# Kernel tuning notes

Measured on AMD Instinct MI355X. Metric: run time of the kernel, lower is better.

## Reference

```python
import jax, jax.numpy as jnp
import numpy as np


def setup_inputs() -> dict:
    key = jax.random.key(0)
    kx, kb, kc, ka = jax.random.split(key, 4)
    batch, seq_len, state_dim = 4, 4096, 1024
    shape = (batch, seq_len, state_dim)
    x = jax.random.normal(kx, shape, dtype=jnp.float32)
    B = jax.random.normal(kb, shape, dtype=jnp.float32)
    C = jax.random.normal(kc, shape, dtype=jnp.float32)
    A = jax.random.uniform(ka, shape, dtype=jnp.float32)  # decay gates in (0,1)
    return {"x": x, "B": B, "C": C, "A": A}


def reference(x, B, C, A):
    # Diagonal selective-scan recurrence: h_t = A_t * h_{t-1} + B_t; y_t = C_t * h_t.
    # x is accepted for interface parity but unused (as in the original module).
    # Scan over time with carry h: [batch, state_dim].
    A_t = jnp.moveaxis(A, 1, 0)  # [seq, batch, dim]
    B_t = jnp.moveaxis(B, 1, 0)
    C_t = jnp.moveaxis(C, 1, 0)
    h0 = jnp.zeros((B.shape[0], B.shape[2]), dtype=B.dtype)

    def step(h, abc):
        a, b, c = abc
        h = a * h + b
        return h, c * h

    _, ys = jax.lax.scan(step, h0, (A_t, B_t, C_t))
    return jnp.moveaxis(ys, 0, 1)  # [batch, seq, dim]
```

## Files before the change

### kernel.cpp

```cpp
#include <hip/hip_runtime.h>

#define BATCH 4
#define SEQ   4096
#define DIM   1024
#define DIM4  (DIM / 4)
#define NC    128
#define CHUNK (SEQ / NC)

__device__ __forceinline__ float4 f4_fma(float4 a, float4 h, float4 b) {
    float4 r;
    r.x = fmaf(a.x, h.x, b.x);
    r.y = fmaf(a.y, h.y, b.y);
    r.z = fmaf(a.z, h.z, b.z);
    r.w = fmaf(a.w, h.w, b.w);
    return r;
}

__device__ __forceinline__ float4 f4_mul(float4 a, float4 b) {
    float4 r;
    r.x = a.x * b.x;
    r.y = a.y * b.y;
    r.z = a.z * b.z;
    r.w = a.w * b.w;
    return r;
}

__global__ __launch_bounds__(256) void ssm_phase1(const float4* __restrict__ A,
                                                  const float4* __restrict__ B,
                                                  float4* __restrict__ P,
                                                  float4* __restrict__ Q) {
    const int c  = blockIdx.x % NC;
    const int b  = blockIdx.x / NC;
    const int d4 = threadIdx.x;

    size_t base = ((size_t)b * SEQ + (size_t)c * CHUNK) * DIM4 + d4;

    float4 p = make_float4(1.f, 1.f, 1.f, 1.f);
    float4 q = make_float4(0.f, 0.f, 0.f, 0.f);

#pragma unroll 8
    for (int t = 0; t < CHUNK; ++t) {
        float4 a  = A[base + (size_t)t * DIM4];
        float4 bb = B[base + (size_t)t * DIM4];
        q = f4_fma(a, q, bb);
        p = f4_mul(p, a);
    }

    size_t w = ((size_t)b * NC + c) * DIM4 + d4;
    P[w] = p;
    Q[w] = q;
}

__global__ __launch_bounds__(256) void ssm_phase2(float4* __restrict__ PH,
                                                  const float4* __restrict__ Q) {
    const int gid = blockIdx.x * 256 + threadIdx.x;
    const int b   = gid / DIM4;
    const int d4  = gid % DIM4;

    float4 h = make_float4(0.f, 0.f, 0.f, 0.f);
    for (int c = 0; c < NC; ++c) {
        size_t idx = ((size_t)b * NC + c) * DIM4 + d4;
        float4 p = PH[idx];
        float4 q = Q[idx];
        PH[idx] = h;
        h = f4_fma(p, h, q);
    }
}

__global__ __launch_bounds__(256) void ssm_phase3(const float4* __restrict__ A,
                                                  const float4* __restrict__ B,
                                                  const float4* __restrict__ C,
                                                  const float4* __restrict__ H,
                                                  float4* __restrict__ Y) {
    const int c  = blockIdx.x % NC;
    const int b  = blockIdx.x / NC;
    const int d4 = threadIdx.x;

    size_t base = ((size_t)b * SEQ + (size_t)c * CHUNK) * DIM4 + d4;

    float4 h = H[((size_t)b * NC + c) * DIM4 + d4];

#pragma unroll 4
    for (int t = 0; t < CHUNK; ++t) {
        float4 a  = A[base + (size_t)t * DIM4];
        float4 bb = B[base + (size_t)t * DIM4];
        float4 cc = C[base + (size_t)t * DIM4];
        h = f4_fma(a, h, bb);
        Y[base + (size_t)t * DIM4] = f4_mul(cc, h);
    }
}

extern "C" void kernel_launch(void* const* d_in, const int* in_sizes, int n_in,
                              void* d_out, int out_size, void* d_ws, size_t ws_size,
                              hipStream_t stream) {
    const float* B = (const float*)d_in[1];
    const float* C = (const float*)d_in[2];
    const float* A = (const float*)d_in[3];
    float* Y = (float*)d_out;

    float* P = (float*)d_ws;
    float* Q = P + (size_t)BATCH * NC * DIM;

    ssm_phase1<<<BATCH * NC, 256, 0, stream>>>(
        (const float4*)A, (const float4*)B, (float4*)P, (float4*)Q);

    ssm_phase2<<<(BATCH * DIM4) / 256, 256, 0, stream>>>(
        (float4*)P, (const float4*)Q);

    ssm_phase3<<<BATCH * NC, 256, 0, stream>>>(
        (const float4*)A, (const float4*)B, (const float4*)C,
        (const float4*)P, (float4*)Y);
}
```

Measured before the change: 86.53 us.

## Use more chunks and a parallel Hillis-Steele scan for chunk carries

Result: slower. 95.29 us (+10.1%).

```diff
diff --git a/kernel.cpp b/kernel.cpp
--- a/kernel.cpp
+++ b/kernel.cpp
@@ -4,7 +4,7 @@
 #define SEQ   4096
 #define DIM   1024
 #define DIM4  (DIM / 4)
-#define NC    128
+#define NC    512
 #define CHUNK (SEQ / NC)
 
 __device__ __forceinline__ float4 f4_fma(float4 a, float4 h, float4 b) {
@@ -38,7 +38,7 @@
     float4 p = make_float4(1.f, 1.f, 1.f, 1.f);
     float4 q = make_float4(0.f, 0.f, 0.f, 0.f);
 
-#pragma unroll 8
+#pragma unroll
     for (int t = 0; t < CHUNK; ++t) {
         float4 a  = A[base + (size_t)t * DIM4];
         float4 bb = B[base + (size_t)t * DIM4];
@@ -51,20 +51,38 @@
     Q[w] = q;
 }
 
-__global__ __launch_bounds__(256) void ssm_phase2(float4* __restrict__ PH,
-                                                  const float4* __restrict__ Q) {
-    const int gid = blockIdx.x * 256 + threadIdx.x;
-    const int b   = gid / DIM4;
-    const int d4  = gid % DIM4;
+__global__ __launch_bounds__(NC) void ssm_phase2(float4* __restrict__ PH,
+                                                 const float4* __restrict__ Q) {
+    const int b  = blockIdx.x / DIM4;
+    const int d4 = blockIdx.x % DIM4;
+    const int c  = threadIdx.x;
 
-    float4 h = make_float4(0.f, 0.f, 0.f, 0.f);
-    for (int c = 0; c < NC; ++c) {
-        size_t idx = ((size_t)b * NC + c) * DIM4 + d4;
-        float4 p = PH[idx];
-        float4 q = Q[idx];
-        PH[idx] = h;
-        h = f4_fma(p, h, q);
+    __shared__ float4 sp[NC];
+    __shared__ float4 sq[NC];
+
+    const size_t idx = ((size_t)b * NC + c) * DIM4 + d4;
+    float4 p = PH[idx];
+    float4 q = Q[idx];
+    sp[c] = p;
+    sq[c] = q;
+    __syncthreads();
+
+    for (int off = 1; off < NC; off <<= 1) {
+        float4 pp, qq;
+        const bool has = (c >= off);
+        if (has) { pp = sp[c - off]; qq = sq[c - off]; }
+        __syncthreads();
+        if (has) {
+            q = f4_fma(p, qq, q);
+            p = f4_mul(p, pp);
+            sp[c] = p;
+            sq[c] = q;
+        }
+        __syncthreads();
     }
+
+    float4 h = (c == 0) ? make_float4(0.f, 0.f, 0.f, 0.f) : sq[c - 1];
+    PH[idx] = h;
 }
 
 __global__ __launch_bounds__(256) void ssm_phase3(const float4* __restrict__ A,
@@ -80,7 +98,7 @@
 
     float4 h = H[((size_t)b * NC + c) * DIM4 + d4];
 
-#pragma unroll 4
+#pragma unroll
     for (int t = 0; t < CHUNK; ++t) {
         float4 a  = A[base + (size_t)t * DIM4];
         float4 bb = B[base + (size_t)t * DIM4];
@@ -104,7 +122,7 @@
     ssm_phase1<<<BATCH * NC, 256, 0, stream>>>(
         (const float4*)A, (const float4*)B, (float4*)P, (float4*)Q);
 
-    ssm_phase2<<<(BATCH * DIM4) / 256, 256, 0, stream>>>(
+    ssm_phase2<<<BATCH * DIM4, NC, 0, stream>>>(
         (float4*)P, (const float4*)Q);
 
     ssm_phase3<<<BATCH * NC, 256, 0, stream>>>(
```
